# Kernel optimization log

Measured on AMD Instinct MI355X. Metric: run time of the kernel, lower is better.

Reference implementation:

```python
import jax, jax.numpy as jnp
import numpy as np

B_, C_, H_, W_ = 4, 256, 64, 64
D_MODEL = C_ // 4        # 64, mamba d_model
D_INNER = 2 * D_MODEL    # 128, expand=2
D_STATE = 16
D_CONV = 4
DT_RANK = 4              # ceil(d_model/16)


def setup_inputs() -> dict:
    key = jax.random.key(0)
    ks = jax.random.split(key, 10)
    s = 0.02
    p = {}
    p["x"] = jax.random.normal(ks[0], (B_, C_, H_, W_), jnp.float32)
    p["norm_g"] = jnp.ones((C_,), jnp.float32)
    p["norm_b"] = jnp.zeros((C_,), jnp.float32)
    p["skip_scale"] = jnp.ones((1,), jnp.float32)
    p["proj_w"] = jax.random.normal(ks[1], (C_, C_), jnp.float32) * s
    p["proj_b"] = jnp.zeros((C_,), jnp.float32)
    p["in_proj_w"] = jax.random.normal(ks[2], (2 * D_INNER, D_MODEL), jnp.float32) * s
    p["conv_w"] = jax.random.normal(ks[3], (D_INNER, 1, D_CONV), jnp.float32) * s
    p["conv_b"] = jnp.zeros((D_INNER,), jnp.float32)
    p["x_proj_w"] = jax.random.normal(ks[4], (DT_RANK + 2 * D_STATE, D_INNER), jnp.float32) * s
    p["dt_w"] = jax.random.normal(ks[5], (D_INNER, DT_RANK), jnp.float32) * s
    p["dt_b"] = jax.random.normal(ks[6], (D_INNER,), jnp.float32) * 0.1
    # S4D-real init: A_n = n for n in 1..d_state
    p["A_log"] = jnp.log(jnp.broadcast_to(jnp.arange(1, D_STATE + 1, dtype=jnp.float32), (D_INNER, D_STATE)))
    p["D"] = jnp.ones((D_INNER,), jnp.float32)
    p["out_w"] = jax.random.normal(ks[7], (D_MODEL, D_INNER), jnp.float32) * s
    return p


def _layernorm(x, g, b, eps=1e-5):
    mu = jnp.mean(x, axis=-1, keepdims=True)
    var = jnp.mean(jnp.square(x - mu), axis=-1, keepdims=True)
    return (x - mu) * jax.lax.rsqrt(var + eps) * g + b


def _mamba(x, in_proj_w, conv_w, conv_b, x_proj_w, dt_w, dt_b, A_log, D, out_w):
    # x: [N, L, d_model]
    N, L, _ = x.shape
    xz = x @ in_proj_w.T                      # [N, L, 2*d_inner]
    xi, z = jnp.split(xz, 2, axis=-1)
    # causal depthwise conv1d over time
    xc = jax.lax.conv_general_dilated(
        xi.transpose(0, 2, 1), conv_w, (1,), [(D_CONV - 1, 0)],
        feature_group_count=D_INNER)          # [N, d_inner, L]
    u = jax.nn.silu((xc + conv_b[None, :, None]).transpose(0, 2, 1))  # [N, L, d_inner]
    dbl = u @ x_proj_w.T                      # [N, L, dt_rank + 2*d_state]
    dt, Bm, Cm = jnp.split(dbl, [DT_RANK, DT_RANK + D_STATE], axis=-1)
    delta = jax.nn.softplus(dt @ dt_w.T + dt_b)  # [N, L, d_inner]
    A = -jnp.exp(A_log)                       # [d_inner, d_state]

    def step(h, inp):
        d_t, B_t, C_t, u_t = inp              # [N,d], [N,n], [N,n], [N,d]
        dA = jnp.exp(d_t[:, :, None] * A)     # [N, d, n]
        h = dA * h + (d_t * u_t)[:, :, None] * B_t[:, None, :]
        y = jnp.einsum('bdn,bn->bd', h, C_t)
        return h, y

    h0 = jnp.zeros((N, D_INNER, D_STATE), x.dtype)
    xs = (delta.transpose(1, 0, 2), Bm.transpose(1, 0, 2),
          Cm.transpose(1, 0, 2), u.transpose(1, 0, 2))
    _, ys = jax.lax.scan(step, h0, xs)        # ys: [L, N, d_inner]
    y = ys.transpose(1, 0, 2) + u * D
    y = y * jax.nn.silu(z)
    return y @ out_w.T                        # [N, L, d_model]


def reference(x, norm_g, norm_b, skip_scale, proj_w, proj_b, in_proj_w, conv_w,
              conv_b, x_proj_w, dt_w, dt_b, A_log, D, out_w):
    B, C = x.shape[:2]
    img_dims = x.shape[2:]
    xf = x.reshape(B, C, -1).transpose(0, 2, 1)       # [B, L, C]
    xn = _layernorm(xf, norm_g, norm_b)
    parts = jnp.split(xn, 8, axis=2)
    b1 = jnp.concatenate([parts[7], parts[0]], axis=2)
    b2 = jnp.concatenate([parts[1], parts[2]], axis=2)
    b3 = jnp.concatenate([parts[3], parts[4]], axis=2)
    b4 = jnp.concatenate([parts[5], parts[6]], axis=2)
    # if_shifted_round=True: all four branches share the same mamba -> batch them
    stacked = jnp.concatenate([b1, b2, b3, b4], axis=0)  # [4B, L, C/4]
    ym = _mamba(stacked, in_proj_w, conv_w, conv_b, x_proj_w,
                dt_w, dt_b, A_log, D, out_w) + skip_scale * stacked
    m1, m2, m3, m4 = jnp.split(ym, 4, axis=0)
    t8, t1 = jnp.split(m1, 2, axis=2)
    xm = jnp.concatenate([t1, m2, m3, m4, t8], axis=2)   # [B, L, C]
    xm = _layernorm(xm, norm_g, norm_b)
    xm = xm @ proj_w.T + proj_b
    return xm.transpose(0, 2, 1).reshape(B, -1, *img_dims)
```

## Files before the change

kernel.cpp:

```cpp
#include <hip/hip_runtime.h>
#include <hip/hip_bf16.h>

#define L_ 4096
#define CCH 256
#define CH 64
#define NC 64

__global__ __launch_bounds__(256) void k1_ln_scatter(
    const float* __restrict__ x, const float* __restrict__ g,
    const float* __restrict__ bb, float* __restrict__ stacked) {
  int b = blockIdx.y;
  int l0 = blockIdx.x * 64;
  int t = threadIdx.x;
  int lane = t & 63, w = t >> 6;
  __shared__ float xs[256][65];
  __shared__ float ps[4][64], ps2[4][64];
  __shared__ float mean_s[64], rstd_s[64];
  for (int i = 0; i < 64; ++i) {
    int c = w + 4 * i;
    xs[c][lane] = x[((size_t)b * 256 + c) * L_ + l0 + lane];
  }
  __syncthreads();
  float sum = 0.f, sq = 0.f;
  for (int c = w * 64; c < w * 64 + 64; ++c) {
    float v = xs[c][lane];
    sum += v; sq += v * v;
  }
  ps[w][lane] = sum; ps2[w][lane] = sq;
  __syncthreads();
  if (w == 0) {
    float s = ps[0][lane] + ps[1][lane] + ps[2][lane] + ps[3][lane];
    float q = ps2[0][lane] + ps2[1][lane] + ps2[2][lane] + ps2[3][lane];
    float mean = s * (1.f / 256.f);
    mean_s[lane] = mean;
    rstd_s[lane] = rsqrtf(q * (1.f / 256.f) - mean * mean + 1e-5f);
  }
  __syncthreads();
  int br = w, j = lane;
  int c = (br * 64 + j + 224) & 255;
  float gv = g[c], bv = bb[c];
  float* dst = stacked + ((size_t)(br * 4 + b) * L_ + l0) * 64 + j;
  for (int l = 0; l < 64; ++l) {
    float v = (xs[c][l] - mean_s[l]) * rstd_s[l] * gv + bv;
    dst[(size_t)l * 64] = v;
  }
}

__global__ __launch_bounds__(256) void k2_inproj(
    const float* __restrict__ stacked, const float* __restrict__ w,
    float* __restrict__ xi, float* __restrict__ z) {
  int n = blockIdx.z, l0 = blockIdx.x * 64, k0 = blockIdx.y * 64;
  __shared__ float As[64][68];
  __shared__ float Ws[64][68];
  int t = threadIdx.y * 16 + threadIdx.x;
  for (int e = t; e < 4096; e += 256) {
    int r = e >> 6, c = e & 63;
    As[r][c] = stacked[((size_t)n * L_ + l0 + r) * 64 + c];
    Ws[r][c] = w[(k0 + r) * 64 + c];
  }
  __syncthreads();
  float acc[4][4] = {};
  for (int jj = 0; jj < 16; ++jj) {
    float4 a[4], bm[4];
#pragma unroll
    for (int i = 0; i < 4; i++) a[i] = *reinterpret_cast<const float4*>(&As[threadIdx.y * 4 + i][jj * 4]);
#pragma unroll
    for (int i = 0; i < 4; i++) bm[i] = *reinterpret_cast<const float4*>(&Ws[threadIdx.x * 4 + i][jj * 4]);
#pragma unroll
    for (int i = 0; i < 4; i++)
#pragma unroll
      for (int kk = 0; kk < 4; kk++)
        acc[i][kk] += a[i].x * bm[kk].x + a[i].y * bm[kk].y + a[i].z * bm[kk].z + a[i].w * bm[kk].w;
  }
  int kb = k0 + threadIdx.x * 4;
  float* dst = (kb < 128) ? xi : z;
  int kd = (kb < 128) ? kb : kb - 128;
#pragma unroll
  for (int i = 0; i < 4; i++) {
    int l = l0 + threadIdx.y * 4 + i;
    float4 v = make_float4(acc[i][0], acc[i][1], acc[i][2], acc[i][3]);
    *reinterpret_cast<float4*>(&dst[((size_t)n * L_ + l) * 128 + kd]) = v;
  }
}

__global__ __launch_bounds__(256) void k3_conv_xproj(
    const float* __restrict__ xi, const float* __restrict__ cw,
    const float* __restrict__ cb, const float* __restrict__ xw,
    const float* __restrict__ dtw, const float* __restrict__ dtb,
    float* __restrict__ u, float* __restrict__ delta,
    float* __restrict__ Bc, float* __restrict__ Cc) {
  int n = blockIdx.y, l0 = blockIdx.x * 64;
  int tid = threadIdx.x;
  __shared__ float us[64][129];
  __shared__ float dbls[64][37];

  {
    int d = tid & 127, lh = tid >> 7;
    int ls = l0 + lh * 32;
    const float* xp = xi + ((size_t)n * L_ + ls) * 128 + d;
    const float4 cwv = *reinterpret_cast<const float4*>(&cw[d * 4]);
    float cbv = cb[d];
    float xm3 = (ls >= 3) ? xp[-3 * 128] : 0.f;
    float xm2 = (ls >= 2) ? xp[-2 * 128] : 0.f;
    float xm1 = (ls >= 1) ? xp[-1 * 128] : 0.f;
    float* up = u + ((size_t)n * L_ + ls) * 128 + d;
#pragma unroll 4
    for (int l = 0; l < 32; ++l) {
      float xv = xp[(size_t)l * 128];
      float s = cbv + cwv.x * xm3 + cwv.y * xm2 + cwv.z * xm1 + cwv.w * xv;
      float uv = s / (1.f + __expf(-s));
      us[lh * 32 + l][d] = uv;
      up[(size_t)l * 128] = uv;
      xm3 = xm2; xm2 = xm1; xm1 = xv;
    }
  }
  __syncthreads();

  {
    int l = tid & 63, q = tid >> 6;
    float acc[9] = {};
    for (int d = 0; d < 128; ++d) {
      float uv = us[l][d];
#pragma unroll
      for (int r = 0; r < 9; ++r) acc[r] += uv * xw[(q * 9 + r) * 128 + d];
    }
#pragma unroll
    for (int r = 0; r < 9; ++r) dbls[l][q * 9 + r] = acc[r];
  }
  __syncthreads();

  {
    int d = tid & 127, lh = tid >> 7;
    const float4 wv = *reinterpret_cast<const float4*>(&dtw[d * 4]);
    float bv = dtb[d];
    float* dp = delta + ((size_t)n * L_ + l0 + lh * 32) * 128 + d;
    for (int l = 0; l < 32; ++l) {
      int lr = lh * 32 + l;
      float q0 = dbls[lr][0], q1 = dbls[lr][1], q2 = dbls[lr][2], q3 = dbls[lr][3];
      float dv = bv + q0 * wv.x + q1 * wv.y + q2 * wv.z + q3 * wv.w;
      dv = (dv > 20.f) ? dv : log1pf(__expf(dv));
      dp[(size_t)l * 128] = dv;
    }
  }

  {
    int s = tid & 15;
    int which = (tid >> 4) & 1;
    int lg = tid >> 5;
    float* dst = which ? Cc : Bc;
    int roff = 4 + which * 16 + s;
    for (int l3 = lg; l3 < 64; l3 += 8) {
      dst[((size_t)n * L_ + l0 + l3) * 16 + s] = dbls[l3][roff];
    }
  }
}

__global__ __launch_bounds__(128) void k4a_chunk(
    const float* __restrict__ delta, const float* __restrict__ u,
    const float* __restrict__ Bc, const float* __restrict__ A_log,
    float* __restrict__ hend, float* __restrict__ Sdelta) {
  int c = blockIdx.x, n = blockIdx.y, d = threadIdx.x;
  __shared__ float Bs[CH * 16];
  const float* bsrc = Bc + ((size_t)n * L_ + c * CH) * 16;
  for (int e = d; e < CH * 16; e += 128) Bs[e] = bsrc[e];
  float A[16];
#pragma unroll
  for (int s = 0; s < 16; ++s) A[s] = -__expf(A_log[d * 16 + s]);
  __syncthreads();

  const float* dp = delta + ((size_t)n * L_ + c * CH) * 128 + d;
  const float* up = u + ((size_t)n * L_ + c * CH) * 128 + d;
  float h[16] = {};
  float sd = 0.f;
  float dv = dp[0], uv = up[0];
  for (int l = 0; l < CH; ++l) {
    int ln = (l + 1 < CH) ? l + 1 : l;
    float dvn = dp[(size_t)ln * 128];
    float uvn = up[(size_t)ln * 128];
    sd += dv;
    float du = dv * uv;
    float bsv[16];
    *reinterpret_cast<float4*>(&bsv[0])  = *reinterpret_cast<const float4*>(&Bs[l * 16 + 0]);
    *reinterpret_cast<float4*>(&bsv[4])  = *reinterpret_cast<const float4*>(&Bs[l * 16 + 4]);
    *reinterpret_cast<float4*>(&bsv[8])  = *reinterpret_cast<const float4*>(&Bs[l * 16 + 8]);
    *reinterpret_cast<float4*>(&bsv[12]) = *reinterpret_cast<const float4*>(&Bs[l * 16 + 12]);
#pragma unroll
    for (int s = 0; s < 16; ++s)
      h[s] = fmaf(__expf(dv * A[s]), h[s], du * bsv[s]);
    dv = dvn; uv = uvn;
  }
  float* hp = hend + (((size_t)n * NC + c) * 128 + d) * 16;
  *reinterpret_cast<float4*>(&hp[0])  = make_float4(h[0], h[1], h[2], h[3]);
  *reinterpret_cast<float4*>(&hp[4])  = make_float4(h[4], h[5], h[6], h[7]);
  *reinterpret_cast<float4*>(&hp[8])  = make_float4(h[8], h[9], h[10], h[11]);
  *reinterpret_cast<float4*>(&hp[12]) = make_float4(h[12], h[13], h[14], h[15]);
  Sdelta[((size_t)n * NC + c) * 128 + d] = sd;
}

__global__ __launch_bounds__(256) void k4b_combine(
    const float* __restrict__ Sdelta, const float* __restrict__ A_log,
    float* __restrict__ hend) {
  int n = blockIdx.x >> 3, d0 = (blockIdx.x & 7) * 16;
  int d = d0 + (threadIdx.x >> 4), s = threadIdx.x & 15;
  float A = -__expf(A_log[d * 16 + s]);
  float H = 0.f;
  size_t i0 = ((size_t)n * NC) * 128 + d;
  float sd = Sdelta[i0];
  float he = hend[i0 * 16 + s];
  for (int c = 0; c < NC; ++c) {
    int cn = (c + 1 < NC) ? c + 1 : c;
    size_t in_ = ((size_t)n * NC + cn) * 128 + d;
    float sdn = Sdelta[in_];
    float hen = hend[in_ * 16 + s];
    size_t i = ((size_t)n * NC + c) * 128 + d;
    hend[i * 16 + s] = H;
    H = fmaf(__expf(A * sd), H, he);
    sd = sdn; he = hen;
  }
}

__global__ __launch_bounds__(128) void k4c_scan(
    const float* __restrict__ delta, const float* __restrict__ u,
    const float* __restrict__ Bc, const float* __restrict__ Cc,
    const float* __restrict__ A_log, const float* __restrict__ Hstart,
    float* __restrict__ y) {
  int c = blockIdx.x, n = blockIdx.y, d = threadIdx.x;
  __shared__ float Bs[CH * 16];
  __shared__ float Cs[CH * 16];
  const float* bsrc = Bc + ((size_t)n * L_ + c * CH) * 16;
  const float* csrc = Cc + ((size_t)n * L_ + c * CH) * 16;
  for (int e = d; e < CH * 16; e += 128) { Bs[e] = bsrc[e]; Cs[e] = csrc[e]; }
  float A[16];
#pragma unroll
  for (int s = 0; s < 16; ++s) A[s] = -__expf(A_log[d * 16 + s]);
  __syncthreads();

  const float* hp = Hstart + (((size_t)n * NC + c) * 128 + d) * 16;
  float h[16];
  *reinterpret_cast<float4*>(&h[0])  = *reinterpret_cast<const float4*>(&hp[0]);
  *reinterpret_cast<float4*>(&h[4])  = *reinterpret_cast<const float4*>(&hp[4]);
  *reinterpret_cast<float4*>(&h[8])  = *reinterpret_cast<const float4*>(&hp[8]);
  *reinterpret_cast<float4*>(&h[12]) = *reinterpret_cast<const float4*>(&hp[12]);

  const float* dp = delta + ((size_t)n * L_ + c * CH) * 128 + d;
  const float* up = u + ((size_t)n * L_ + c * CH) * 128 + d;
  float* yp = y + ((size_t)n * L_ + c * CH) * 128 + d;
  float dv = dp[0], uv = up[0];
  for (int l = 0; l < CH; ++l) {
    int ln = (l + 1 < CH) ? l + 1 : l;
    float dvn = dp[(size_t)ln * 128];
    float uvn = up[(size_t)ln * 128];
    float du = dv * uv;
    float bsv[16], csv[16];
    *reinterpret_cast<float4*>(&bsv[0])  = *reinterpret_cast<const float4*>(&Bs[l * 16 + 0]);
    *reinterpret_cast<float4*>(&bsv[4])  = *reinterpret_cast<const float4*>(&Bs[l * 16 + 4]);
    *reinterpret_cast<float4*>(&bsv[8])  = *reinterpret_cast<const float4*>(&Bs[l * 16 + 8]);
    *reinterpret_cast<float4*>(&bsv[12]) = *reinterpret_cast<const float4*>(&Bs[l * 16 + 12]);
    *reinterpret_cast<float4*>(&csv[0])  = *reinterpret_cast<const float4*>(&Cs[l * 16 + 0]);
    *reinterpret_cast<float4*>(&csv[4])  = *reinterpret_cast<const float4*>(&Cs[l * 16 + 4]);
    *reinterpret_cast<float4*>(&csv[8])  = *reinterpret_cast<const float4*>(&Cs[l * 16 + 8]);
    *reinterpret_cast<float4*>(&csv[12]) = *reinterpret_cast<const float4*>(&Cs[l * 16 + 12]);
    float yv = 0.f;
#pragma unroll
    for (int s = 0; s < 16; ++s) {
      h[s] = fmaf(__expf(dv * A[s]), h[s], du * bsv[s]);
      yv = fmaf(h[s], csv[s], yv);
    }
    yp[(size_t)l * 128] = yv;
    dv = dvn; uv = uvn;
  }
}

__global__ __launch_bounds__(256) void k5_gate_outproj(
    const float* __restrict__ y, const float* __restrict__ u,
    const float* __restrict__ z, const float* __restrict__ Dv,
    const float* __restrict__ ow, const float* __restrict__ stacked,
    const float* __restrict__ skip, float* __restrict__ ym) {
  int n = blockIdx.y, l0 = blockIdx.x * 64;
  __shared__ float As[64][132];
  __shared__ float Ws[64][132];
  int t = threadIdx.y * 16 + threadIdx.x;
  for (int e = t; e < 64 * 128; e += 256) {
    int r = e >> 7, c = e & 127;
    size_t idx = ((size_t)n * L_ + l0 + r) * 128 + c;
    float zz = z[idx];
    As[r][c] = (y[idx] + u[idx] * Dv[c]) * (zz / (1.f + __expf(-zz)));
    Ws[r][c] = ow[(size_t)r * 128 + c];
  }
  __syncthreads();
  float acc[4][4] = {};
  for (int jj = 0; jj < 32; ++jj) {
    float4 a[4], bm[4];
#pragma unroll
    for (int i = 0; i < 4; i++) a[i] = *reinterpret_cast<const float4*>(&As[threadIdx.y * 4 + i][jj * 4]);
#pragma unroll
    for (int i = 0; i < 4; i++) bm[i] = *reinterpret_cast<const float4*>(&Ws[threadIdx.x * 4 + i][jj * 4]);
#pragma unroll
    for (int i = 0; i < 4; i++)
#pragma unroll
      for (int kk = 0; kk < 4; kk++)
        acc[i][kk] += a[i].x * bm[kk].x + a[i].y * bm[kk].y + a[i].z * bm[kk].z + a[i].w * bm[kk].w;
  }
  float sk = skip[0];
#pragma unroll
  for (int i = 0; i < 4; i++) {
    int l = l0 + threadIdx.y * 4 + i;
    const float4 st = *reinterpret_cast<const float4*>(&stacked[((size_t)n * L_ + l) * 64 + threadIdx.x * 4]);
    float4 v = make_float4(acc[i][0] + sk * st.x, acc[i][1] + sk * st.y,
                           acc[i][2] + sk * st.z, acc[i][3] + sk * st.w);
    *reinterpret_cast<float4*>(&ym[((size_t)n * L_ + l) * 64 + threadIdx.x * 4]) = v;
  }
}

__global__ __launch_bounds__(256) void k6a_ln2(
    const float* __restrict__ ym, const float* __restrict__ g,
    const float* __restrict__ bb, float* __restrict__ xmn) {
  int b = blockIdx.y;
  int l = blockIdx.x * 4 + (threadIdx.x >> 6);
  int j = threadIdx.x & 63;
  float v[4];
  float sum = 0.f, sq = 0.f;
#pragma unroll
  for (int br = 0; br < 4; ++br) {
    v[br] = ym[((size_t)(br * 4 + b) * L_ + l) * 64 + j];
    sum += v[br]; sq += v[br] * v[br];
  }
#pragma unroll
  for (int off = 1; off < 64; off <<= 1) {
    sum += __shfl_xor(sum, off);
    sq  += __shfl_xor(sq, off);
  }
  float mean = sum * (1.f / 256.f);
  float rstd = rsqrtf(sq * (1.f / 256.f) - mean * mean + 1e-5f);
#pragma unroll
  for (int br = 0; br < 4; ++br) {
    int c = (br * 64 + j + 224) & 255;
    xmn[((size_t)b * L_ + l) * 256 + c] = (v[br] - mean) * rstd * g[c] + bb[c];
  }
}

__global__ __launch_bounds__(256) void k6b_proj(
    const float* __restrict__ xmn, const float* __restrict__ pw,
    const float* __restrict__ pb, float* __restrict__ out) {
  int b = blockIdx.z, k0 = blockIdx.y * 64, l0 = blockIdx.x * 64;
  __shared__ float As[64][68];
  __shared__ float Ws[64][68];
  int t = threadIdx.y * 16 + threadIdx.x;
  float acc[4][4] = {};
  for (int cc = 0; cc < 4; ++cc) {
    __syncthreads();
    for (int e = t; e < 4096; e += 256) {
      int r = e >> 6, c = e & 63;
      As[r][c] = xmn[((size_t)b * L_ + l0 + r) * 256 + cc * 64 + c];
      Ws[r][c] = pw[(k0 + r) * 256 + cc * 64 + c];
    }
    __syncthreads();
    for (int jj = 0; jj < 16; ++jj) {
      float4 a[4], bm[4];
#pragma unroll
      for (int i = 0; i < 4; i++) a[i] = *reinterpret_cast<const float4*>(&As[threadIdx.y * 4 + i][jj * 4]);
#pragma unroll
      for (int i = 0; i < 4; i++) bm[i] = *reinterpret_cast<const float4*>(&Ws[threadIdx.x * 4 + i][jj * 4]);
#pragma unroll
      for (int i = 0; i < 4; i++)
#pragma unroll
        for (int kk = 0; kk < 4; kk++)
          acc[i][kk] += a[i].x * bm[kk].x + a[i].y * bm[kk].y + a[i].z * bm[kk].z + a[i].w * bm[kk].w;
    }
  }
  __syncthreads();
  float* Ct = &As[0][0];
#pragma unroll
  for (int i = 0; i < 4; i++)
#pragma unroll
    for (int kk = 0; kk < 4; kk++)
      Ct[(threadIdx.y * 4 + i) * 65 + (threadIdx.x * 4 + kk)] = acc[i][kk];
  __syncthreads();
  int lane64 = t & 63, w = t >> 6;
#pragma unroll
  for (int p = 0; p < 16; ++p) {
    int row = p * 4 + w;
    out[((size_t)b * 256 + k0 + row) * L_ + l0 + lane64] = Ct[lane64 * 65 + row] + pb[k0 + row];
  }
}

extern "C" void kernel_launch(void* const* d_in, const int* in_sizes, int n_in,
                              void* d_out, int out_size, void* d_ws, size_t ws_size,
                              hipStream_t stream) {
  const float* x        = (const float*)d_in[0];
  const float* norm_g   = (const float*)d_in[1];
  const float* norm_b   = (const float*)d_in[2];
  const float* skip     = (const float*)d_in[3];
  const float* proj_w   = (const float*)d_in[4];
  const float* proj_b   = (const float*)d_in[5];
  const float* in_proj_w= (const float*)d_in[6];
  const float* conv_w   = (const float*)d_in[7];
  const float* conv_b   = (const float*)d_in[8];
  const float* x_proj_w = (const float*)d_in[9];
  const float* dt_w     = (const float*)d_in[10];
  const float* dt_b     = (const float*)d_in[11];
  const float* A_log    = (const float*)d_in[12];
  const float* Dv       = (const float*)d_in[13];
  const float* out_w    = (const float*)d_in[14];
  float* out = (float*)d_out;
  float* ws  = (float*)d_ws;

  float* stacked = ws;
  float* xi      = ws + 4194304;
  float* z       = ws + 12582912;
  float* u       = ws + 20971520;
  float* delta   = ws + 29360128;
  float* Bc      = ws + 37748736;
  float* Cc      = ws + 38797312;
  float* ym      = delta;
  float* xmn     = delta + 4194304;

  float* hend   = out;
  float* Sdelta = out + 2097152;

  k1_ln_scatter<<<dim3(64, 4), 256, 0, stream>>>(x, norm_g, norm_b, stacked);
  k2_inproj<<<dim3(64, 4, 16), dim3(16, 16), 0, stream>>>(stacked, in_proj_w, xi, z);
  k3_conv_xproj<<<dim3(64, 16), 256, 0, stream>>>(xi, conv_w, conv_b, x_proj_w,
                                                  dt_w, dt_b, u, delta, Bc, Cc);
  k4a_chunk<<<dim3(NC, 16), 128, 0, stream>>>(delta, u, Bc, A_log, hend, Sdelta);
  k4b_combine<<<128, 256, 0, stream>>>(Sdelta, A_log, hend);
  k4c_scan<<<dim3(NC, 16), 128, 0, stream>>>(delta, u, Bc, Cc, A_log, hend, xi );
  k5_gate_outproj<<<dim3(64, 16), dim3(16, 16), 0, stream>>>(xi , u, z, Dv,
                                                             out_w, stacked, skip, ym);
  k6a_ln2<<<dim3(1024, 4), 256, 0, stream>>>(ym, norm_g, norm_b, xmn);
  k6b_proj<<<dim3(64, 4, 4), dim3(16, 16), 0, stream>>>(xmn, proj_w, proj_b, out);
}
```

Baseline: 403.5 us.

## Fuse chunk scan with gating/out-proj and LayerNorm2 with final projection

Merges the chunked selective scan with the D-skip, SiLU gate and out-projection GEMM, so the scan result goes straight into shared memory instead of a global y buffer. Also fuses the second LayerNorm into the final projection kernel, which computes per-row statistics and normalizes while loading tiles, removing the xmn intermediate. This cuts global round trips and two launches. In exchange only half the threads in the fused scan block run the serial scan while the rest wait, and LN statistics are recomputed by each of the 4 output-channel blocks.

```diff
diff --git a/kernel.cpp b/kernel.cpp
--- a/kernel.cpp
+++ b/kernel.cpp
@@ -219,82 +219,80 @@
   }
 }
 
-__global__ __launch_bounds__(128) void k4c_scan(
+__global__ __launch_bounds__(256) void k45_scan_gate_proj(
     const float* __restrict__ delta, const float* __restrict__ u,
     const float* __restrict__ Bc, const float* __restrict__ Cc,
     const float* __restrict__ A_log, const float* __restrict__ Hstart,
-    float* __restrict__ y) {
-  int c = blockIdx.x, n = blockIdx.y, d = threadIdx.x;
-  __shared__ float Bs[CH * 16];
-  __shared__ float Cs[CH * 16];
-  const float* bsrc = Bc + ((size_t)n * L_ + c * CH) * 16;
-  const float* csrc = Cc + ((size_t)n * L_ + c * CH) * 16;
-  for (int e = d; e < CH * 16; e += 128) { Bs[e] = bsrc[e]; Cs[e] = csrc[e]; }
-  float A[16];
-#pragma unroll
-  for (int s = 0; s < 16; ++s) A[s] = -__expf(A_log[d * 16 + s]);
-  __syncthreads();
-
-  const float* hp = Hstart + (((size_t)n * NC + c) * 128 + d) * 16;
-  float h[16];
-  *reinterpret_cast<float4*>(&h[0])  = *reinterpret_cast<const float4*>(&hp[0]);
-  *reinterpret_cast<float4*>(&h[4])  = *reinterpret_cast<const float4*>(&hp[4]);
-  *reinterpret_cast<float4*>(&h[8])  = *reinterpret_cast<const float4*>(&hp[8]);
-  *reinterpret_cast<float4*>(&h[12]) = *reinterpret_cast<const float4*>(&hp[12]);
-
-  const float* dp = delta + ((size_t)n * L_ + c * CH) * 128 + d;
-  const float* up = u + ((size_t)n * L_ + c * CH) * 128 + d;
-  float* yp = y + ((size_t)n * L_ + c * CH) * 128 + d;
-  float dv = dp[0], uv = up[0];
-  for (int l = 0; l < CH; ++l) {
-    int ln = (l + 1 < CH) ? l + 1 : l;
-    float dvn = dp[(size_t)ln * 128];
-    float uvn = up[(size_t)ln * 128];
-    float du = dv * uv;
-    float bsv[16], csv[16];
-    *reinterpret_cast<float4*>(&bsv[0])  = *reinterpret_cast<const float4*>(&Bs[l * 16 + 0]);
-    *reinterpret_cast<float4*>(&bsv[4])  = *reinterpret_cast<const float4*>(&Bs[l * 16 + 4]);
-    *reinterpret_cast<float4*>(&bsv[8])  = *reinterpret_cast<const float4*>(&Bs[l * 16 + 8]);
-    *reinterpret_cast<float4*>(&bsv[12]) = *reinterpret_cast<const float4*>(&Bs[l * 16 + 12]);
-    *reinterpret_cast<float4*>(&csv[0])  = *reinterpret_cast<const float4*>(&Cs[l * 16 + 0]);
-    *reinterpret_cast<float4*>(&csv[4])  = *reinterpret_cast<const float4*>(&Cs[l * 16 + 4]);
-    *reinterpret_cast<float4*>(&csv[8])  = *reinterpret_cast<const float4*>(&Cs[l * 16 + 8]);
-    *reinterpret_cast<float4*>(&csv[12]) = *reinterpret_cast<const float4*>(&Cs[l * 16 + 12]);
-    float yv = 0.f;
-#pragma unroll
-    for (int s = 0; s < 16; ++s) {
-      h[s] = fmaf(__expf(dv * A[s]), h[s], du * bsv[s]);
-      yv = fmaf(h[s], csv[s], yv);
-    }
-    yp[(size_t)l * 128] = yv;
-    dv = dvn; uv = uvn;
-  }
-}
-
-__global__ __launch_bounds__(256) void k5_gate_outproj(
-    const float* __restrict__ y, const float* __restrict__ u,
     const float* __restrict__ z, const float* __restrict__ Dv,
     const float* __restrict__ ow, const float* __restrict__ stacked,
     const float* __restrict__ skip, float* __restrict__ ym) {
-  int n = blockIdx.y, l0 = blockIdx.x * 64;
+  int c = blockIdx.x, n = blockIdx.y;
+  int tid = threadIdx.x;
   __shared__ float As[64][132];
   __shared__ float Ws[64][132];
-  int t = threadIdx.y * 16 + threadIdx.x;
-  for (int e = t; e < 64 * 128; e += 256) {
-    int r = e >> 7, c = e & 127;
-    size_t idx = ((size_t)n * L_ + l0 + r) * 128 + c;
-    float zz = z[idx];
-    As[r][c] = (y[idx] + u[idx] * Dv[c]) * (zz / (1.f + __expf(-zz)));
-    Ws[r][c] = ow[(size_t)r * 128 + c];
-  }
-  __syncthreads();
+  __shared__ float Bs[CH * 16];
+  __shared__ float Cs[CH * 16];
+
+  const float* bsrc = Bc + ((size_t)n * L_ + c * CH) * 16;
+  const float* csrc = Cc + ((size_t)n * L_ + c * CH) * 16;
+  for (int e = tid; e < CH * 16; e += 256) { Bs[e] = bsrc[e]; Cs[e] = csrc[e]; }
+  for (int e = tid; e < 64 * 128; e += 256) {
+    int r = e >> 7, d = e & 127;
+    Ws[r][d] = ow[(size_t)r * 128 + d];
+  }
+  __syncthreads();
+
+  if (tid < 128) {
+    int d = tid;
+    float A[16];
+#pragma unroll
+    for (int s = 0; s < 16; ++s) A[s] = -__expf(A_log[d * 16 + s]);
+    const float* hp = Hstart + (((size_t)n * NC + c) * 128 + d) * 16;
+    float h[16];
+    *reinterpret_cast<float4*>(&h[0])  = *reinterpret_cast<const float4*>(&hp[0]);
+    *reinterpret_cast<float4*>(&h[4])  = *reinterpret_cast<const float4*>(&hp[4]);
+    *reinterpret_cast<float4*>(&h[8])  = *reinterpret_cast<const float4*>(&hp[8]);
+    *reinterpret_cast<float4*>(&h[12]) = *reinterpret_cast<const float4*>(&hp[12]);
+    const float* dp = delta + ((size_t)n * L_ + c * CH) * 128 + d;
+    const float* up = u + ((size_t)n * L_ + c * CH) * 128 + d;
+    const float* zp = z + ((size_t)n * L_ + c * CH) * 128 + d;
+    float Dd = Dv[d];
+    float dv = dp[0], uv = up[0], zv = zp[0];
+    for (int l = 0; l < CH; ++l) {
+      int ln = (l + 1 < CH) ? l + 1 : l;
+      float dvn = dp[(size_t)ln * 128];
+      float uvn = up[(size_t)ln * 128];
+      float zvn = zp[(size_t)ln * 128];
+      float du = dv * uv;
+      float bsv[16], csv[16];
+      *reinterpret_cast<float4*>(&bsv[0])  = *reinterpret_cast<const float4*>(&Bs[l * 16 + 0]);
+      *reinterpret_cast<float4*>(&bsv[4])  = *reinterpret_cast<const float4*>(&Bs[l * 16 + 4]);
+      *reinterpret_cast<float4*>(&bsv[8])  = *reinterpret_cast<const float4*>(&Bs[l * 16 + 8]);
+      *reinterpret_cast<float4*>(&bsv[12]) = *reinterpret_cast<const float4*>(&Bs[l * 16 + 12]);
+      *reinterpret_cast<float4*>(&csv[0])  = *reinterpret_cast<const float4*>(&Cs[l * 16 + 0]);
+      *reinterpret_cast<float4*>(&csv[4])  = *reinterpret_cast<const float4*>(&Cs[l * 16 + 4]);
+      *reinterpret_cast<float4*>(&csv[8])  = *reinterpret_cast<const float4*>(&Cs[l * 16 + 8]);
+      *reinterpret_cast<float4*>(&csv[12]) = *reinterpret_cast<const float4*>(&Cs[l * 16 + 12]);
+      float yv = 0.f;
+#pragma unroll
+      for (int s = 0; s < 16; ++s) {
+        h[s] = fmaf(__expf(dv * A[s]), h[s], du * bsv[s]);
+        yv = fmaf(h[s], csv[s], yv);
+      }
+      As[l][d] = (yv + uv * Dd) * (zv / (1.f + __expf(-zv)));
+      dv = dvn; uv = uvn; zv = zvn;
+    }
+  }
+  __syncthreads();
+
+  int tx = tid & 15, ty = tid >> 4;
   float acc[4][4] = {};
   for (int jj = 0; jj < 32; ++jj) {
     float4 a[4], bm[4];
 #pragma unroll
-    for (int i = 0; i < 4; i++) a[i] = *reinterpret_cast<const float4*>(&As[threadIdx.y * 4 + i][jj * 4]);
-#pragma unroll
-    for (int i = 0; i < 4; i++) bm[i] = *reinterpret_cast<const float4*>(&Ws[threadIdx.x * 4 + i][jj * 4]);
+    for (int i = 0; i < 4; i++) a[i] = *reinterpret_cast<const float4*>(&As[ty * 4 + i][jj * 4]);
+#pragma unroll
+    for (int i = 0; i < 4; i++) bm[i] = *reinterpret_cast<const float4*>(&Ws[tx * 4 + i][jj * 4]);
 #pragma unroll
     for (int i = 0; i < 4; i++)
 #pragma unroll
@@ -302,57 +300,60 @@
         acc[i][kk] += a[i].x * bm[kk].x + a[i].y * bm[kk].y + a[i].z * bm[kk].z + a[i].w * bm[kk].w;
   }
   float sk = skip[0];
+  int l0 = c * CH;
 #pragma unroll
   for (int i = 0; i < 4; i++) {
-    int l = l0 + threadIdx.y * 4 + i;
-    const float4 st = *reinterpret_cast<const float4*>(&stacked[((size_t)n * L_ + l) * 64 + threadIdx.x * 4]);
+    int l = l0 + ty * 4 + i;
+    const float4 st = *reinterpret_cast<const float4*>(&stacked[((size_t)n * L_ + l) * 64 + tx * 4]);
     float4 v = make_float4(acc[i][0] + sk * st.x, acc[i][1] + sk * st.y,
                            acc[i][2] + sk * st.z, acc[i][3] + sk * st.w);
-    *reinterpret_cast<float4*>(&ym[((size_t)n * L_ + l) * 64 + threadIdx.x * 4]) = v;
-  }
-}
-
-__global__ __launch_bounds__(256) void k6a_ln2(
+    *reinterpret_cast<float4*>(&ym[((size_t)n * L_ + l) * 64 + tx * 4]) = v;
+  }
+}
+
+__global__ __launch_bounds__(256) void k6_ln_proj(
     const float* __restrict__ ym, const float* __restrict__ g,
-    const float* __restrict__ bb, float* __restrict__ xmn) {
-  int b = blockIdx.y;
-  int l = blockIdx.x * 4 + (threadIdx.x >> 6);
-  int j = threadIdx.x & 63;
-  float v[4];
-  float sum = 0.f, sq = 0.f;
-#pragma unroll
-  for (int br = 0; br < 4; ++br) {
-    v[br] = ym[((size_t)(br * 4 + b) * L_ + l) * 64 + j];
-    sum += v[br]; sq += v[br] * v[br];
-  }
-#pragma unroll
-  for (int off = 1; off < 64; off <<= 1) {
-    sum += __shfl_xor(sum, off);
-    sq  += __shfl_xor(sq, off);
-  }
-  float mean = sum * (1.f / 256.f);
-  float rstd = rsqrtf(sq * (1.f / 256.f) - mean * mean + 1e-5f);
-#pragma unroll
-  for (int br = 0; br < 4; ++br) {
-    int c = (br * 64 + j + 224) & 255;
-    xmn[((size_t)b * L_ + l) * 256 + c] = (v[br] - mean) * rstd * g[c] + bb[c];
-  }
-}
-
-__global__ __launch_bounds__(256) void k6b_proj(
-    const float* __restrict__ xmn, const float* __restrict__ pw,
+    const float* __restrict__ bb, const float* __restrict__ pw,
     const float* __restrict__ pb, float* __restrict__ out) {
   int b = blockIdx.z, k0 = blockIdx.y * 64, l0 = blockIdx.x * 64;
   __shared__ float As[64][68];
   __shared__ float Ws[64][68];
+  __shared__ float mean_s[64], rstd_s[64];
   int t = threadIdx.y * 16 + threadIdx.x;
+  int lane = t & 63, w = t >> 6;
+
+  for (int li = w; li < 64; li += 4) {
+    int l = l0 + li;
+    float sum = 0.f, sq = 0.f;
+#pragma unroll
+    for (int br = 0; br < 4; ++br) {
+      float v = ym[((size_t)(br * 4 + b) * L_ + l) * 64 + lane];
+      sum += v; sq += v * v;
+    }
+#pragma unroll
+    for (int off = 1; off < 64; off <<= 1) {
+      sum += __shfl_xor(sum, off);
+      sq  += __shfl_xor(sq, off);
+    }
+    if (lane == 0) {
+      float mean = sum * (1.f / 256.f);
+      mean_s[li] = mean;
+      rstd_s[li] = rsqrtf(sq * (1.f / 256.f) - mean * mean + 1e-5f);
+    }
+  }
+  __syncthreads();
+
   float acc[4][4] = {};
   for (int cc = 0; cc < 4; ++cc) {
     __syncthreads();
     for (int e = t; e < 4096; e += 256) {
-      int r = e >> 6, c = e & 63;
-      As[r][c] = xmn[((size_t)b * L_ + l0 + r) * 256 + cc * 64 + c];
-      Ws[r][c] = pw[(k0 + r) * 256 + cc * 64 + c];
+      int r = e >> 6, cj = e & 63;
+      int ch = cc * 64 + cj;
+      int gi = (ch + 32) & 255;
+      int br = gi >> 6, j = gi & 63;
+      float v = ym[((size_t)(br * 4 + b) * L_ + l0 + r) * 64 + j];
+      As[r][cj] = (v - mean_s[r]) * rstd_s[r] * g[ch] + bb[ch];
+      Ws[r][cj] = pw[(k0 + r) * 256 + ch];
     }
     __syncthreads();
     for (int jj = 0; jj < 16; ++jj) {
@@ -376,11 +377,10 @@
     for (int kk = 0; kk < 4; kk++)
       Ct[(threadIdx.y * 4 + i) * 65 + (threadIdx.x * 4 + kk)] = acc[i][kk];
   __syncthreads();
-  int lane64 = t & 63, w = t >> 6;
 #pragma unroll
   for (int p = 0; p < 16; ++p) {
     int row = p * 4 + w;
-    out[((size_t)b * 256 + k0 + row) * L_ + l0 + lane64] = Ct[lane64 * 65 + row] + pb[k0 + row];
+    out[((size_t)b * 256 + k0 + row) * L_ + l0 + lane] = Ct[lane * 65 + row] + pb[k0 + row];
   }
 }
 
@@ -412,8 +412,7 @@
   float* delta   = ws + 29360128;
   float* Bc      = ws + 37748736;
   float* Cc      = ws + 38797312;
-  float* ym      = delta;
-  float* xmn     = delta + 4194304;
+  float* ym      = xi;
 
   float* hend   = out;
   float* Sdelta = out + 2097152;
@@ -424,9 +423,8 @@
                                                   dt_w, dt_b, u, delta, Bc, Cc);
   k4a_chunk<<<dim3(NC, 16), 128, 0, stream>>>(delta, u, Bc, A_log, hend, Sdelta);
   k4b_combine<<<128, 256, 0, stream>>>(Sdelta, A_log, hend);
-  k4c_scan<<<dim3(NC, 16), 128, 0, stream>>>(delta, u, Bc, Cc, A_log, hend, xi );
-  k5_gate_outproj<<<dim3(64, 16), dim3(16, 16), 0, stream>>>(xi , u, z, Dv,
-                                                             out_w, stacked, skip, ym);
-  k6a_ln2<<<dim3(1024, 4), 256, 0, stream>>>(ym, norm_g, norm_b, xmn);
-  k6b_proj<<<dim3(64, 4, 4), dim3(16, 16), 0, stream>>>(xmn, proj_w, proj_b, out);
-}
+  k45_scan_gate_proj<<<dim3(NC, 16), 256, 0, stream>>>(delta, u, Bc, Cc, A_log, hend,
+                                                       z, Dv, out_w, stacked, skip, ym);
+  k6_ln_proj<<<dim3(64, 4, 4), dim3(16, 16), 0, stream>>>(ym, norm_g, norm_b,
+                                                          proj_w, proj_b, out);
+}
```

Result: slower. 414.1 us (+2.6%).
